# Kernel optimization log

Hardware: AMD Instinct MI355X
Metric: run time of the kernel (lower is better)

Reference implementation:

```python
import jax, jax.numpy as jnp
import numpy as np

EPS = 1e-6

def _rms_norm(x, w):
    # per-head RMSNorm over last dim (head_dim)
    var = jnp.mean(jnp.square(x), axis=-1, keepdims=True)
    return x * jax.lax.rsqrt(var + EPS) * w

def _linear(x, w, b):
    # torch nn.Linear: y = x @ W^T + b
    return jnp.einsum('bsd,od->bso', x, w) + b

def setup_inputs() -> dict:
    key = jax.random.key(0)
    ks = jax.random.split(key, 16)
    B, S, S_enc, D, H, HD = 1, 2048, 256, 1536, 24, 64
    w = lambda k: jax.random.normal(k, (D, D), dtype=jnp.float32) * 0.02
    return {
        'hidden_states': jax.random.normal(ks[0], (B, S, D), dtype=jnp.float32),
        'encoder_hidden_states': jax.random.normal(ks[1], (B, S_enc, D), dtype=jnp.float32),
        'attention_mask': jnp.zeros((B, 1, 1, S + S_enc), dtype=jnp.float32),
        'to_q_weight': w(ks[2]), 'to_q_bias': jnp.zeros((D,), jnp.float32),
        'to_k_weight': w(ks[3]), 'to_k_bias': jnp.zeros((D,), jnp.float32),
        'to_v_weight': w(ks[4]), 'to_v_bias': jnp.zeros((D,), jnp.float32),
        'norm_q_weight': jnp.ones((HD,), jnp.float32),
        'norm_k_weight': jnp.ones((HD,), jnp.float32),
        'add_q_proj_weight': w(ks[5]), 'add_q_proj_bias': jnp.zeros((D,), jnp.float32),
        'add_k_proj_weight': w(ks[6]), 'add_k_proj_bias': jnp.zeros((D,), jnp.float32),
        'add_v_proj_weight': w(ks[7]), 'add_v_proj_bias': jnp.zeros((D,), jnp.float32),
        'norm_added_q_weight': jnp.ones((HD,), jnp.float32),
        'norm_added_k_weight': jnp.ones((HD,), jnp.float32),
        'to_out_0_weight': w(ks[8]), 'to_out_0_bias': jnp.zeros((D,), jnp.float32),
        'to_add_out_weight': w(ks[9]), 'to_add_out_bias': jnp.zeros((D,), jnp.float32),
        'attn_heads': 24,
        'attn_head_dim': 64,
    }

def reference(hidden_states, encoder_hidden_states, attention_mask,
              to_q_weight, to_q_bias, to_k_weight, to_k_bias, to_v_weight, to_v_bias,
              norm_q_weight, norm_k_weight,
              add_q_proj_weight, add_q_proj_bias, add_k_proj_weight, add_k_proj_bias,
              add_v_proj_weight, add_v_proj_bias,
              norm_added_q_weight, norm_added_k_weight,
              to_out_0_weight, to_out_0_bias, to_add_out_weight, to_add_out_bias,
              attn_heads, attn_head_dim):
    B, S, D = hidden_states.shape
    S_enc = encoder_hidden_states.shape[1]
    H, HD = attn_heads, attn_head_dim
    scale = float(HD) ** -0.5

    def split_heads(x):  # [B,T,H*HD] -> [B,H,T,HD]
        return x.reshape(B, -1, H, HD).transpose(0, 2, 1, 3)

    # hidden-stream QKV + per-head RMSNorm on q,k
    q = _rms_norm(split_heads(_linear(hidden_states, to_q_weight, to_q_bias)), norm_q_weight)
    k = _rms_norm(split_heads(_linear(hidden_states, to_k_weight, to_k_bias)), norm_k_weight)
    v = split_heads(_linear(hidden_states, to_v_weight, to_v_bias))

    # encoder-stream QKV + per-head RMSNorm on q,k
    eq = _rms_norm(split_heads(_linear(encoder_hidden_states, add_q_proj_weight, add_q_proj_bias)), norm_added_q_weight)
    ek = _rms_norm(split_heads(_linear(encoder_hidden_states, add_k_proj_weight, add_k_proj_bias)), norm_added_k_weight)
    ev = split_heads(_linear(encoder_hidden_states, add_v_proj_weight, add_v_proj_bias))

    # concat streams along sequence: [B,H,S+S_enc,HD]
    q = jnp.concatenate([q, eq], axis=2)
    k = jnp.concatenate([k, ek], axis=2)
    v = jnp.concatenate([v, ev], axis=2)

    # SDPA with additive mask
    scores = jnp.einsum('bhqd,bhkd->bhqk', q, k) * scale + attention_mask
    probs = jax.nn.softmax(scores, axis=-1)
    out = jnp.einsum('bhqk,bhkd->bhqd', probs, v)  # [B,H,T,HD]
    out = out.transpose(0, 2, 1, 3).reshape(B, S + S_enc, H * HD)

    # split back into image / text streams, separate output projections
    attn_output = _linear(out[:, :S], to_out_0_weight, to_out_0_bias)
    context_attn_output = _linear(out[:, S:], to_add_out_weight, to_add_out_bias)
    del context_attn_output  # AttentionFunc returns only the hidden-stream output
    return attn_output
```

## Files before the change

### kernel.cpp

```cpp
#include <hip/hip_runtime.h>
#include <cstdint>


typedef __attribute__((ext_vector_type(8))) short s16x8;
typedef __attribute__((ext_vector_type(4))) float f32x4;

#define LOG2E 1.4426950408889634f

__device__ __forceinline__ short f2bf(float f) {
  union { float f; uint32_t u; } v; v.f = f;
  uint32_t r = v.u + 0x7FFFu + ((v.u >> 16) & 1u);
  return (short)(r >> 16);
}

__device__ __forceinline__ uint32_t cvt_pk_bf16(float lo, float hi) {
  uint32_t r;
  asm("v_cvt_pk_bf16_f32 %0, %1, %2" : "=v"(r) : "v"(lo), "v"(hi));
  return r;
}

typedef uint32_t __attribute__((address_space(1)))* gas_u32;
typedef uint32_t __attribute__((address_space(3)))* las_u32;

__device__ __forceinline__ void gload_lds16(const short* g, short* l) {
  __builtin_amdgcn_global_load_lds((gas_u32)(g), (las_u32)(l), 16, 0, 0);
}

struct CvtSeg { const float* src; short* dst; int n4; };
struct CvtArgs { CvtSeg s[8]; const float* msrc; float* mdst; int mn4; };

__global__ __launch_bounds__(256) void cvt_bf16_kernel(CvtArgs a) {
  const int stride = gridDim.x * blockDim.x;
  const int tid = blockIdx.x * blockDim.x + threadIdx.x;
  for (int i = 0; i < 8; ++i) {
    const float4* src = (const float4*)a.s[i].src;
    short* dst = a.s[i].dst;
    const int n4 = a.s[i].n4;
    for (int j = tid; j < n4; j += stride) {
      float4 v = src[j];
      short4 o;
      o.x = f2bf(v.x); o.y = f2bf(v.y); o.z = f2bf(v.z); o.w = f2bf(v.w);
      *(short4*)(dst + (size_t)j * 4) = o;
    }
  }
  const float4* ms = (const float4*)a.msrc;
  float4* md = (float4*)a.mdst;
  for (int j = tid; j < a.mn4; j += stride) {
    float4 m = ms[j];
    float4 o = {m.x * LOG2E, m.y * LOG2E, m.z * LOG2E, m.w * LOG2E};
    md[j] = o;
  }
}

enum { MODE_Q = 0, MODE_K = 1, MODE_V = 2, MODE_OUT = 3 };

struct GemmCfg {
  const short* A;
  const short* W;
  const float* bias;
  const float* normw;
  void* dst;
  int toff;
  int mode;
  int mtiles;
};
struct GemmArgs { GemmCfg c[5]; };

__global__ __launch_bounds__(256) void proj_gemm_kernel(GemmArgs args, int chunk) {
  const int w = (blockIdx.x & 7) * chunk + (blockIdx.x >> 3);
  int z, tx, ty;
  if (w < 576) { z = w / 192; const int r = w % 192; tx = r >> 4; ty = r & 15; }
  else { int r = w - 576; z = 3 + r / 24; r %= 24; tx = r >> 1; ty = r & 1; }
  const GemmCfg cfg = args.c[z];
  constexpr int K = 1536;
  __shared__ short As[4096];
  __shared__ short Bs[4096];
  const int t = threadIdx.x;
  const int lane = t & 63;
  const int wave = t >> 6;
  const int l16 = lane & 15;
  const int quad = lane >> 4;
  const int wm = wave >> 1;
  const int wn = wave & 1;

  const short* __restrict__ Ag = cfg.A + (size_t)(ty * 128) * K;
  const short* __restrict__ Wg = cfg.W + (size_t)(tx * 128) * K;
  const int srow = t >> 2;
  const int scol = (t & 3) << 3;

  const f32x4 z4 = {0.f, 0.f, 0.f, 0.f};
  f32x4 acc[4][4];
#pragma unroll
  for (int i = 0; i < 4; ++i) {
#pragma unroll
    for (int j = 0; j < 4; ++j) acc[i][j] = z4;
  }

  for (int k0 = 0; k0 < K; k0 += 32) {
    gload_lds16(Ag + (size_t)srow * K + k0 + scol, As + t * 8);
    gload_lds16(Ag + (size_t)(srow + 64) * K + k0 + scol, As + 2048 + t * 8);
    gload_lds16(Wg + (size_t)srow * K + k0 + scol, Bs + t * 8);
    gload_lds16(Wg + (size_t)(srow + 64) * K + k0 + scol, Bs + 2048 + t * 8);
    __syncthreads();
    s16x8 af[4], bfr[4];
#pragma unroll
    for (int i = 0; i < 4; ++i)
      af[i] = *(const s16x8*)(As + (wm * 64 + i * 16 + l16) * 32 + quad * 8);
#pragma unroll
    for (int i = 0; i < 4; ++i)
      bfr[i] = *(const s16x8*)(Bs + (wn * 64 + i * 16 + l16) * 32 + quad * 8);
#pragma unroll
    for (int mi = 0; mi < 4; ++mi) {
#pragma unroll
      for (int ni = 0; ni < 4; ++ni)
        acc[mi][ni] = __builtin_amdgcn_mfma_f32_16x16x32_bf16(af[mi], bfr[ni], acc[mi][ni], 0, 0, 0);
    }
    __syncthreads();
  }

  const int nbase = tx * 128 + wn * 64;
  const int mbase = ty * 128 + wm * 64;
  const int mode = cfg.mode;
  const int h = nbase >> 6;

  float biasv[4], nwv[4];
#pragma unroll
  for (int ni = 0; ni < 4; ++ni) {
    int col = nbase + ni * 16 + l16;
    biasv[ni] = cfg.bias[col];
    nwv[ni] = (mode == MODE_Q || mode == MODE_K) ? cfg.normw[col & 63] : 0.f;
  }

#pragma unroll
  for (int mi = 0; mi < 4; ++mi) {
    float vv[4][4];
#pragma unroll
    for (int ni = 0; ni < 4; ++ni) {
#pragma unroll
      for (int r = 0; r < 4; ++r) vv[ni][r] = acc[mi][ni][r] + biasv[ni];
    }
    if (mode == MODE_Q || mode == MODE_K) {
      float ss[4];
#pragma unroll
      for (int r = 0; r < 4; ++r)
        ss[r] = vv[0][r] * vv[0][r] + vv[1][r] * vv[1][r] +
                vv[2][r] * vv[2][r] + vv[3][r] * vv[3][r];
#pragma unroll
      for (int r = 0; r < 4; ++r) {
        ss[r] += __shfl_xor(ss[r], 1);
        ss[r] += __shfl_xor(ss[r], 2);
        ss[r] += __shfl_xor(ss[r], 4);
        ss[r] += __shfl_xor(ss[r], 8);
        float rs = rsqrtf(ss[r] * (1.0f / 64.0f) + 1e-6f);
#pragma unroll
        for (int ni = 0; ni < 4; ++ni) vv[ni][r] *= rs * nwv[ni];
      }
    }
    const int row0 = mbase + mi * 16 + quad * 4;
    if (mode == MODE_Q) {
      short* Qd = (short*)cfg.dst;
#pragma unroll
      for (int ni = 0; ni < 4; ++ni) {
        int d = ni * 16 + l16;
#pragma unroll
        for (int r = 0; r < 4; ++r)
          Qd[((size_t)h * 2048 + row0 + r) * 64 + d] = f2bf(vv[ni][r]);
      }
    } else if (mode == MODE_K) {
      short* Kd = (short*)cfg.dst;
#pragma unroll
      for (int ni = 0; ni < 4; ++ni) {
        int d = ni * 16 + l16;
#pragma unroll
        for (int r = 0; r < 4; ++r)
          Kd[((size_t)h * 2304 + cfg.toff + row0 + r) * 64 + d] = f2bf(vv[ni][r]);
      }
    } else if (mode == MODE_V) {
      short* Vd = (short*)cfg.dst;
#pragma unroll
      for (int ni = 0; ni < 4; ++ni) {
        int d = ni * 16 + l16;
        short4 o4;
        o4.x = f2bf(vv[ni][0]); o4.y = f2bf(vv[ni][1]);
        o4.z = f2bf(vv[ni][2]); o4.w = f2bf(vv[ni][3]);
        *(short4*)(Vd + ((size_t)h * 64 + d) * 2304 + cfg.toff + row0) = o4;
      }
    } else {
      float* Od = (float*)cfg.dst;
#pragma unroll
      for (int ni = 0; ni < 4; ++ni) {
        int col = nbase + ni * 16 + l16;
#pragma unroll
        for (int r = 0; r < 4; ++r)
          Od[(size_t)(row0 + r) * 1536 + col] = vv[ni][r];
      }
    }
  }
}

__global__ __launch_bounds__(256) void flash_kernel(
    const short* __restrict__ Q, const short* __restrict__ Kc,
    const short* __restrict__ VT, const float* __restrict__ mlt,
    short* __restrict__ AO) {
  const int b = blockIdx.x;
  const int h = (b & 7) * 3 + ((b >> 3) % 3);
  const int q0 = ((b >> 3) / 3) * 64;
  const int lane = threadIdx.x & 63;
  const int wave = threadIdx.x >> 6;
  const int qw = wave & 1;
  const int ks = wave >> 1;
  const int l16 = lane & 15;
  const int quad = lane >> 4;

  __shared__ __align__(16) short smem[16384];

  const short* Kh = Kc + (size_t)h * 2304 * 64;
  const short* Vh = VT + (size_t)h * 64 * 2304;

  s16x8 aq0[2], aq1[2];
#pragma unroll
  for (int g = 0; g < 2; ++g) {
    const short* Qrow =
        Q + ((size_t)h * 2048 + q0 + qw * 32 + g * 16 + l16) * 64;
    aq0[g] = *(const s16x8*)(Qrow + quad * 8);
    aq1[g] = *(const s16x8*)(Qrow + quad * 8 + 32);
  }

  s16x8 ones;
#pragma unroll
  for (int i = 0; i < 8; ++i) ones[i] = (short)0x3F80;

  const f32x4 z4 = {0.f, 0.f, 0.f, 0.f};
  f32x4 o[2][4];
#pragma unroll
  for (int g = 0; g < 2; ++g)
#pragma unroll
    for (int mi = 0; mi < 4; ++mi) o[g][mi] = z4;
  f32x4 lacc[2] = {z4, z4};
  const float SC = 0.125f * LOG2E;
  const int kbase = ks * 1152;

  const int gi0 = qw * 64 + lane;
  const int trow0 = gi0 >> 3, cp0 = gi0 & 7;
  const int srow0 = ((trow0 & 12) << 1) | (trow0 & 3);
  const int d0 = gi0 >> 2, cpv0 = gi0 & 3;
  const short* kS = Kh + (size_t)kbase * 64 + srow0 * 64 + ((cp0 ^ (trow0 & 7)) << 3);
  const short* vS = Vh + (size_t)d0 * 2304 + kbase + ((cpv0 ^ ((d0 >> 1) & 3)) << 3);
  const int ldst = qw * 512 + lane * 8;

  auto stage = [&](int it, int buf) {
    short* kt = smem + (ks * 2 + buf) * 2048;
    short* vt = smem + 8192 + (ks * 2 + buf) * 2048;
    const short* ksrc = kS + it * 2048;
    const short* vsrc = vS + it * 32;
    gload_lds16(ksrc,             kt + ldst);
    gload_lds16(ksrc + 256,       kt + 1024 + ldst);
    gload_lds16(vsrc,             vt + ldst);
    gload_lds16(vsrc + 32 * 2304, vt + 1024 + ldst);
  };

  stage(0, 0);
  __syncthreads();

#pragma unroll 2
  for (int it = 0; it < 36; ++it) {
    const int buf = it & 1;
    if (it < 35) stage(it + 1, buf ^ 1);
    const short* kt = smem + (ks * 2 + buf) * 2048;
    const short* vt = smem + 8192 + (ks * 2 + buf) * 2048;
    const int kb = kbase + it * 32;

    s16x8 bk[2][2];
#pragma unroll
    for (int ni = 0; ni < 2; ++ni) {
      const int tt = ni * 16 + l16;
      const short* kr = kt + tt * 64;
      bk[ni][0] = *(const s16x8*)(kr + ((quad ^ (tt & 7)) << 3));
      bk[ni][1] = *(const s16x8*)(kr + (((quad + 4) ^ (tt & 7)) << 3));
    }
    s16x8 bv[4];
#pragma unroll
    for (int mi = 0; mi < 4; ++mi) {
      const int d = mi * 16 + l16;
      bv[mi] = *(const s16x8*)(vt + d * 32 + ((quad ^ ((d >> 1) & 3)) << 3));
    }
    float4 mv0 = *(const float4*)(mlt + kb + quad * 8);
    float4 mv1 = *(const float4*)(mlt + kb + quad * 8 + 4);
    const float m8[8] = {mv0.x, mv0.y, mv0.z, mv0.w, mv1.x, mv1.y, mv1.z, mv1.w};

#pragma unroll
    for (int g = 0; g < 2; ++g) {
      union { uint32_t w[4]; s16x8 v; } pu;
#pragma unroll
      for (int ni = 0; ni < 2; ++ni) {
        f32x4 s = __builtin_amdgcn_mfma_f32_16x16x32_bf16(bk[ni][0], aq0[g], z4, 0, 0, 0);
        s = __builtin_amdgcn_mfma_f32_16x16x32_bf16(bk[ni][1], aq1[g], s, 0, 0, 0);
        float p[4];
#pragma unroll
        for (int rr = 0; rr < 4; ++rr)
          p[rr] = __builtin_amdgcn_exp2f(fmaf(s[rr], SC, m8[ni * 4 + rr]));
        pu.w[ni * 2 + 0] = cvt_pk_bf16(p[0], p[1]);
        pu.w[ni * 2 + 1] = cvt_pk_bf16(p[2], p[3]);
      }
      lacc[g] = __builtin_amdgcn_mfma_f32_16x16x32_bf16(pu.v, ones, lacc[g], 0, 0, 0);
#pragma unroll
      for (int mi = 0; mi < 4; ++mi)
        o[g][mi] = __builtin_amdgcn_mfma_f32_16x16x32_bf16(pu.v, bv[mi], o[g][mi], 0, 0, 0);
    }
    __syncthreads();
  }

  f32x4* R = (f32x4*)smem;
  if (ks == 1) {
    f32x4* Rw = R + (qw * 64 + lane) * 10;
#pragma unroll
    for (int g = 0; g < 2; ++g) {
#pragma unroll
      for (int mi = 0; mi < 4; ++mi) Rw[g * 5 + mi] = o[g][mi];
      Rw[g * 5 + 4] = lacc[g];
    }
  }
  __syncthreads();
  if (ks == 0) {
    const f32x4* Rw = R + (qw * 64 + lane) * 10;
#pragma unroll
    for (int g = 0; g < 2; ++g) {
#pragma unroll
      for (int mi = 0; mi < 4; ++mi) o[g][mi] += Rw[g * 5 + mi];
      f32x4 lt = lacc[g] + Rw[g * 5 + 4];
#pragma unroll
      for (int rr = 0; rr < 4; ++rr) {
        float inv = 1.0f / lt[rr];
        int tq = q0 + qw * 32 + g * 16 + quad * 4 + rr;
#pragma unroll
        for (int mi = 0; mi < 4; ++mi)
          AO[(size_t)tq * 1536 + h * 64 + mi * 16 + l16] = f2bf(o[g][mi][rr] * inv);
      }
    }
  }
}

extern "C" void kernel_launch(void* const* d_in, const int* in_sizes, int n_in,
                              void* d_out, int out_size, void* d_ws, size_t ws_size,
                              hipStream_t stream) {
  (void)in_sizes; (void)n_in; (void)out_size; (void)ws_size;
  const float* hidden = (const float*)d_in[0];
  const float* enc    = (const float*)d_in[1];
  const float* amask  = (const float*)d_in[2];
  const float* wq  = (const float*)d_in[3];  const float* bq  = (const float*)d_in[4];
  const float* wk  = (const float*)d_in[5];  const float* bk  = (const float*)d_in[6];
  const float* wv  = (const float*)d_in[7];  const float* bv  = (const float*)d_in[8];
  const float* nqw = (const float*)d_in[9];  const float* nkw = (const float*)d_in[10];
  const float* wak = (const float*)d_in[13]; const float* bak = (const float*)d_in[14];
  const float* wav = (const float*)d_in[15]; const float* bav = (const float*)d_in[16];
  const float* nakw = (const float*)d_in[18];
  const float* wo  = (const float*)d_in[19]; const float* bo  = (const float*)d_in[20];
  float* out = (float*)d_out;

  char* p = (char*)d_ws;
  auto carve = [&](size_t bytes) { char* r = p; p += (bytes + 255) & ~(size_t)255; return r; };
  short* Xb   = (short*)carve((size_t)2048 * 1536 * 2);
  short* Eb   = (short*)carve((size_t)256 * 1536 * 2);
  short* Wqb  = (short*)carve((size_t)1536 * 1536 * 2);
  short* Wkb  = (short*)carve((size_t)1536 * 1536 * 2);
  short* Wvb  = (short*)carve((size_t)1536 * 1536 * 2);
  short* Wakb = (short*)carve((size_t)1536 * 1536 * 2);
  short* Wavb = (short*)carve((size_t)1536 * 1536 * 2);
  short* Wob  = (short*)carve((size_t)1536 * 1536 * 2);
  short* Qb   = (short*)carve((size_t)24 * 2048 * 64 * 2);
  short* Kb   = (short*)carve((size_t)24 * 2304 * 64 * 2);
  short* VTb  = (short*)carve((size_t)24 * 64 * 2304 * 2);
  short* AOb  = (short*)carve((size_t)2048 * 1536 * 2);
  float* MLb  = (float*)carve((size_t)2304 * 4);

  CvtArgs ca;
  ca.s[0] = {hidden, Xb, 2048 * 1536 / 4};
  ca.s[1] = {enc,    Eb, 256 * 1536 / 4};
  ca.s[2] = {wq,  Wqb,  1536 * 1536 / 4};
  ca.s[3] = {wk,  Wkb,  1536 * 1536 / 4};
  ca.s[4] = {wv,  Wvb,  1536 * 1536 / 4};
  ca.s[5] = {wak, Wakb, 1536 * 1536 / 4};
  ca.s[6] = {wav, Wavb, 1536 * 1536 / 4};
  ca.s[7] = {wo,  Wob,  1536 * 1536 / 4};
  ca.msrc = amask; ca.mdst = MLb; ca.mn4 = 2304 / 4;
  cvt_bf16_kernel<<<dim3(1024), dim3(256), 0, stream>>>(ca);

  GemmArgs g1;
  g1.c[0] = {Xb, Wqb,  bq,  nqw,     (void*)Qb,  0,    MODE_Q, 16};
  g1.c[1] = {Xb, Wkb,  bk,  nkw,     (void*)Kb,  0,    MODE_K, 16};
  g1.c[2] = {Xb, Wvb,  bv,  nullptr, (void*)VTb, 0,    MODE_V, 16};
  g1.c[3] = {Eb, Wakb, bak, nakw,    (void*)Kb,  2048, MODE_K, 2};
  g1.c[4] = {Eb, Wavb, bav, nullptr, (void*)VTb, 2048, MODE_V, 2};
  proj_gemm_kernel<<<dim3(624), dim3(256), 0, stream>>>(g1, 78);

  flash_kernel<<<dim3(768), dim3(256), 0, stream>>>(Qb, Kb, VTb, MLb, AOb);

  GemmArgs g3;
  g3.c[0] = {AOb, Wob, bo, nullptr, (void*)out, 0, MODE_OUT, 16};
  proj_gemm_kernel<<<dim3(192), dim3(256), 0, stream>>>(g3, 24);
}
```

Baseline: 279.8 us.

## Double-buffer LDS tiles and XOR-swizzle layout in projection GEMM

The projection GEMM now keeps two LDS buffers and issues the global-to-LDS loads for the next K slice before computing on the current one, overlapping memory latency with MFMA work. It also applies an XOR swizzle to the column offset when writing and reading the tiles to reduce LDS bank conflicts on the fragment reads. Shared memory per block doubles, which may reduce occupancy, and the unused mtiles field is renamed to padding.

```diff
diff --git a/kernel.cpp b/kernel.cpp
--- a/kernel.cpp
+++ b/kernel.cpp
@@ -62,7 +62,7 @@
   void* dst;
   int toff;
   int mode;
-  int mtiles;
+  int pad;
 };
 struct GemmArgs { GemmCfg c[5]; };
 
@@ -73,8 +73,8 @@
   else { int r = w - 576; z = 3 + r / 24; r %= 24; tx = r >> 1; ty = r & 1; }
   const GemmCfg cfg = args.c[z];
   constexpr int K = 1536;
-  __shared__ short As[4096];
-  __shared__ short Bs[4096];
+  __shared__ short As[8192];
+  __shared__ short Bs[8192];
   const int t = threadIdx.x;
   const int lane = t & 63;
   const int wave = t >> 6;
@@ -86,7 +86,7 @@
   const short* __restrict__ Ag = cfg.A + (size_t)(ty * 128) * K;
   const short* __restrict__ Wg = cfg.W + (size_t)(tx * 128) * K;
   const int srow = t >> 2;
-  const int scol = (t & 3) << 3;
+  const int ssw = ((t & 3) ^ ((srow >> 1) & 3)) << 3;
 
   const f32x4 z4 = {0.f, 0.f, 0.f, 0.f};
   f32x4 acc[4][4];
@@ -96,19 +96,34 @@
     for (int j = 0; j < 4; ++j) acc[i][j] = z4;
   }
 
-  for (int k0 = 0; k0 < K; k0 += 32) {
-    gload_lds16(Ag + (size_t)srow * K + k0 + scol, As + t * 8);
-    gload_lds16(Ag + (size_t)(srow + 64) * K + k0 + scol, As + 2048 + t * 8);
-    gload_lds16(Wg + (size_t)srow * K + k0 + scol, Bs + t * 8);
-    gload_lds16(Wg + (size_t)(srow + 64) * K + k0 + scol, Bs + 2048 + t * 8);
-    __syncthreads();
+  auto stage = [&](int it, int buf) {
+    const int k0 = it * 32;
+    short* a = As + buf * 4096;
+    short* b = Bs + buf * 4096;
+    gload_lds16(Ag + (size_t)srow * K + k0 + ssw, a + t * 8);
+    gload_lds16(Ag + (size_t)(srow + 64) * K + k0 + ssw, a + 2048 + t * 8);
+    gload_lds16(Wg + (size_t)srow * K + k0 + ssw, b + t * 8);
+    gload_lds16(Wg + (size_t)(srow + 64) * K + k0 + ssw, b + 2048 + t * 8);
+  };
+
+  stage(0, 0);
+  __syncthreads();
+
+  const int rsw = (quad ^ ((l16 >> 1) & 3)) << 3;
+
+#pragma unroll 2
+  for (int it = 0; it < 48; ++it) {
+    const int buf = it & 1;
+    if (it < 47) stage(it + 1, buf ^ 1);
+    const short* a = As + buf * 4096;
+    const short* b = Bs + buf * 4096;
     s16x8 af[4], bfr[4];
 #pragma unroll
     for (int i = 0; i < 4; ++i)
-      af[i] = *(const s16x8*)(As + (wm * 64 + i * 16 + l16) * 32 + quad * 8);
+      af[i] = *(const s16x8*)(a + (wm * 64 + i * 16 + l16) * 32 + rsw);
 #pragma unroll
     for (int i = 0; i < 4; ++i)
-      bfr[i] = *(const s16x8*)(Bs + (wn * 64 + i * 16 + l16) * 32 + quad * 8);
+      bfr[i] = *(const s16x8*)(b + (wn * 64 + i * 16 + l16) * 32 + rsw);
 #pragma unroll
     for (int mi = 0; mi < 4; ++mi) {
 #pragma unroll
@@ -386,16 +401,16 @@
   cvt_bf16_kernel<<<dim3(1024), dim3(256), 0, stream>>>(ca);
 
   GemmArgs g1;
-  g1.c[0] = {Xb, Wqb,  bq,  nqw,     (void*)Qb,  0,    MODE_Q, 16};
-  g1.c[1] = {Xb, Wkb,  bk,  nkw,     (void*)Kb,  0,    MODE_K, 16};
-  g1.c[2] = {Xb, Wvb,  bv,  nullptr, (void*)VTb, 0,    MODE_V, 16};
-  g1.c[3] = {Eb, Wakb, bak, nakw,    (void*)Kb,  2048, MODE_K, 2};
-  g1.c[4] = {Eb, Wavb, bav, nullptr, (void*)VTb, 2048, MODE_V, 2};
+  g1.c[0] = {Xb, Wqb,  bq,  nqw,     (void*)Qb,  0,    MODE_Q, 0};
+  g1.c[1] = {Xb, Wkb,  bk,  nkw,     (void*)Kb,  0,    MODE_K, 0};
+  g1.c[2] = {Xb, Wvb,  bv,  nullptr, (void*)VTb, 0,    MODE_V, 0};
+  g1.c[3] = {Eb, Wakb, bak, nakw,    (void*)Kb,  2048, MODE_K, 0};
+  g1.c[4] = {Eb, Wavb, bav, nullptr, (void*)VTb, 2048, MODE_V, 0};
   proj_gemm_kernel<<<dim3(624), dim3(256), 0, stream>>>(g1, 78);
 
   flash_kernel<<<dim3(768), dim3(256), 0, stream>>>(Qb, Kb, VTb, MLb, AOb);
 
   GemmArgs g3;
-  g3.c[0] = {AOb, Wob, bo, nullptr, (void*)out, 0, MODE_OUT, 16};
+  g3.c[0] = {AOb, Wob, bo, nullptr, (void*)out, 0, MODE_OUT, 0};
   proj_gemm_kernel<<<dim3(192), dim3(256), 0, stream>>>(g3, 24);
 }
```

After: 302.8 us. 8.2% more time.
